# Kernel tuning notes

Measured on AMD Instinct MI355X. Metric: run time of the kernel, lower is better.

## Reference

```python
import jax, jax.numpy as jnp
import numpy as np

NUM_HEADS = 16
HEAD_DIM = 64
HIDDEN = NUM_HEADS * HEAD_DIM  # 1024
MAX_POS = 1024


def setup_inputs() -> dict:
    key = jax.random.key(0)
    ks = jax.random.split(key, 6)
    B, L, H = 8, 1024, HIDDEN
    hidden_states = jax.random.normal(ks[0], (B, L, H), dtype=jnp.float32)
    attention_mask = jnp.zeros((B, 1, 1, L), dtype=jnp.float32)
    scale = 0.02  # keep pre-softmax logits in a sane range
    Wq = jax.random.normal(ks[1], (H, H), dtype=jnp.float32) * scale
    Wk = jax.random.normal(ks[2], (H, H), dtype=jnp.float32) * scale
    Wv = jax.random.normal(ks[3], (H, H), dtype=jnp.float32) * scale
    bq = jnp.zeros((H,), dtype=jnp.float32)
    bk = jnp.zeros((H,), dtype=jnp.float32)
    bv = jnp.zeros((H,), dtype=jnp.float32)
    dist_emb = jax.random.normal(ks[4], (2 * MAX_POS - 1, HEAD_DIM), dtype=jnp.float32) * scale
    return {"hidden_states": hidden_states, "attention_mask": attention_mask,
            "Wq": Wq, "bq": bq, "Wk": Wk, "bk": bk, "Wv": Wv, "bv": bv,
            "dist_emb": dist_emb}


def _split_heads(x):
    # [B, L, H] -> [B, nH, L, hd]
    B, L, _ = x.shape
    return x.reshape(B, L, NUM_HEADS, HEAD_DIM).transpose(0, 2, 1, 3)


def reference(hidden_states, attention_mask, Wq, bq, Wk, bk, Wv, bv, dist_emb):
    B, L, H = hidden_states.shape
    q = _split_heads(hidden_states @ Wq.T + bq)  # [B,h,L,d]
    k = _split_heads(hidden_states @ Wk.T + bk)
    v = _split_heads(hidden_states @ Wv.T + bv)

    scores = jnp.einsum("bhld,bhrd->bhlr", q, k)

    # relative_key_query positional bias
    pos_l = jnp.arange(L)[:, None]
    pos_r = jnp.arange(L)[None, :]
    dist_idx = pos_l - pos_r + MAX_POS - 1          # [L, L], in [0, 2*MAX_POS-2]
    pos_emb = dist_emb[dist_idx]                    # [L, L, d]
    scores = scores + jnp.einsum("bhld,lrd->bhlr", q, pos_emb)
    scores = scores + jnp.einsum("bhrd,lrd->bhlr", k, pos_emb)

    scores = scores / jnp.sqrt(jnp.float32(HEAD_DIM))
    scores = scores + attention_mask                # additive mask broadcast [B,1,1,L]
    probs = jax.nn.softmax(scores, axis=-1)         # dropout = identity (eval)
    ctx = jnp.einsum("bhlr,bhrd->bhld", probs, v)
    ctx = ctx.transpose(0, 2, 1, 3).reshape(B, L, H)
    return ctx
```

## Files before the change

kernel.cpp:

```cpp
#include <hip/hip_runtime.h>
#include <stdint.h>

typedef short s16x8 __attribute__((ext_vector_type(8)));
typedef float f32x4 __attribute__((ext_vector_type(4)));

#define MFMA16(a, b, c) __builtin_amdgcn_mfma_f32_16x16x32_bf16((a), (b), (c), 0, 0, 0)

__device__ __forceinline__ ushort f2b(float f) {
  union { float f; uint32_t u; } x; x.f = f;
  uint32_t r = x.u + 0x7fffu + ((x.u >> 16) & 1u);
  return (ushort)(r >> 16);
}
__device__ __forceinline__ float b2f(ushort s) {
  union { uint32_t u; float f; } x; x.u = ((uint32_t)s) << 16;
  return x.f;
}
__device__ __forceinline__ uint32_t pack2t(float a, float b) {
  return __builtin_amdgcn_perm(__float_as_uint(b), __float_as_uint(a), 0x07060302u);
}

__global__ __launch_bounds__(256) void cast_f32_bf16(const float* __restrict__ src,
                                                     ushort* __restrict__ dst, int n) {
  int i = (blockIdx.x * 256 + threadIdx.x) * 4;
  if (i + 4 <= n) {
    float4 v = *(const float4*)(src + i);
    ushort4 o; o.x = f2b(v.x); o.y = f2b(v.y); o.z = f2b(v.z); o.w = f2b(v.w);
    *(ushort4*)(dst + i) = o;
  }
}

__device__ __forceinline__ void gload16(const void* g, void* l) {
  __builtin_amdgcn_global_load_lds((const __attribute__((address_space(1))) void*)g,
                                   (__attribute__((address_space(3))) void*)l, 16, 0, 0);
}

__global__ __launch_bounds__(256) void qkv_gemm(
    const ushort* __restrict__ hb, const ushort* __restrict__ wb,
    const float* __restrict__ bq, const float* __restrict__ bk, const float* __restrict__ bv,
    ushort* __restrict__ qb, ushort* __restrict__ kb, ushort* __restrict__ vt) {
  __shared__ ushort As[128 * 32];
  __shared__ ushort Bs[128 * 32];
  const int tid = threadIdx.x;
  const int w = tid >> 6, lane = tid & 63, quad = lane >> 4, l16 = lane & 15;
  const int m0 = blockIdx.y * 128, n0 = blockIdx.x * 128;

  const int srow = w * 32 + (lane >> 2);
  const int scol = (lane & 3) * 8;
  const ushort* ga = hb + (size_t)(m0 + srow) * 1024 + scol;
  const ushort* gw = wb + (size_t)(n0 + srow) * 1024 + scol;
  ushort* lA0 = As + (w * 32) * 32;
  ushort* lA1 = As + (w * 32 + 16) * 32;
  ushort* lB0 = Bs + (w * 32) * 32;
  ushort* lB1 = Bs + (w * 32 + 16) * 32;

  f32x4 acc[4][4];
#pragma unroll
  for (int mt = 0; mt < 4; ++mt)
#pragma unroll
    for (int nt = 0; nt < 4; ++nt) acc[mt][nt] = (f32x4){0.f, 0.f, 0.f, 0.f};

  const int wm = (w >> 1) * 64, wn = (w & 1) * 64;

  for (int k0 = 0; k0 < 1024; k0 += 32) {
    gload16(ga + k0, lA0);
    gload16(ga + k0 + 16 * 1024, lA1);
    gload16(gw + k0, lB0);
    gload16(gw + k0 + 16 * 1024, lB1);
    __syncthreads();
    s16x8 af[4], bfr[4];
#pragma unroll
    for (int mt = 0; mt < 4; ++mt)
      af[mt] = *(const s16x8*)(As + (wm + 16 * mt + l16) * 32 + quad * 8);
#pragma unroll
    for (int nt = 0; nt < 4; ++nt)
      bfr[nt] = *(const s16x8*)(Bs + (wn + 16 * nt + l16) * 32 + quad * 8);
#pragma unroll
    for (int mt = 0; mt < 4; ++mt)
#pragma unroll
      for (int nt = 0; nt < 4; ++nt)
        acc[mt][nt] = MFMA16(af[mt], bfr[nt], acc[mt][nt]);
    __syncthreads();
  }

  const int mat = n0 >> 10;
  const float* bias = (mat == 0) ? bq : ((mat == 1) ? bk : bv);
  const int b = m0 >> 10;
#pragma unroll
  for (int mt = 0; mt < 4; ++mt) {
    int mbase = m0 + wm + 16 * mt + 4 * quad;
#pragma unroll
    for (int nt = 0; nt < 4; ++nt) {
      int n = n0 + wn + 16 * nt + l16;
      int o = n & 1023; int hh = o >> 6; int d = o & 63;
      float bsv = bias[o];
#pragma unroll
      for (int reg = 0; reg < 4; ++reg) {
        int l = (mbase + reg) & 1023;
        ushort bx = f2b(acc[mt][nt][reg] + bsv);
        if (mat == 0)      qb[(((size_t)(b * 16 + hh)) * 1024 + l) * 64 + d] = bx;
        else if (mat == 1) kb[(((size_t)(b * 16 + hh)) * 1024 + l) * 64 + d] = bx;
        else               vt[(((size_t)(b * 16 + hh)) * 64 + d) * 1024 + l] = bx;
      }
    }
  }
}

#define KR  0
#define VR  8192
#define ER  16384
#define SER 28672
#define PR  35072

__device__ __forceinline__ const s16x8* fragp(const ushort* base, int row, int cb) {
  return (const s16x8*)(base + row * 64 + ((cb ^ (row & 7)) * 8));
}

__global__ __launch_bounds__(256, 2) void attn_kernel(
    const ushort* __restrict__ qb, const ushort* __restrict__ kb,
    const ushort* __restrict__ vt, const ushort* __restrict__ eb,
    const float* __restrict__ mask, float* __restrict__ out) {
  __shared__ __align__(16) ushort sm[39168];
  const int tid = threadIdx.x;
  const int w = tid >> 6, lane = tid & 63, quad = lane >> 4, l16 = lane & 15;
  const int bh = blockIdx.y, b = bh >> 4, h = bh & 15;
  const int l0 = blockIdx.x * 64;

  const int srow = lane >> 3;
  const int colb = ((lane & 7) ^ srow) * 8;
  const int row0 = w * 8 + srow;

  const ushort* kp = kb + ((size_t)bh * 1024 + row0) * 64 + colb;
  const ushort* vp = vt + ((size_t)bh * 64 + row0) * 1024 + colb;
  const float* maskp = mask + b * 1024 + l16;

  const int p0 = blockIdx.x % 3;

  {
    const ushort* qp = qb + ((size_t)bh * 1024 + l0 + row0) * 64 + colb;
    gload16(qp,         sm + PR + w * 512);
    gload16(qp + 2048,  sm + PR + 2048 + w * 512);
    gload16(kp,         sm + KR + w * 512);
    gload16(kp + 2048,  sm + KR + 2048 + w * 512);
    gload16(vp,         sm + VR + w * 512);
    gload16(vp + 32768, sm + VR + 2048 + w * 512);
    const int t0i = l0 + 960;
#pragma unroll
    for (int c2 = 0; c2 < 4; ++c2) {
      int jb = w * 8 + 32 * c2;
      int seg = p0 + (jb >> 6); if (seg >= 3) seg -= 3;
      int t = t0i + jb + srow; if (t > 2046) t = 2046;
      gload16(eb + (size_t)t * 64 + colb, sm + ER + seg * 4096 + (jb & 63) * 64);
    }
  }
  __syncthreads();

  s16x8 aq0, aq1;
  {
    int r = w * 16 + l16;
    aq0 = *fragp(sm + PR, r, quad);
    aq1 = *fragp(sm + PR, r, quad + 4);
  }

  float rsum[4];
  f32x4 o_acc[4];
#pragma unroll
  for (int r = 0; r < 4; ++r) rsum[r] = 0.f;
#pragma unroll
  for (int nt = 0; nt < 4; ++nt) o_acc[nt] = (f32x4){0.f, 0.f, 0.f, 0.f};

  const float LOG2E = 1.44269504088896f;
  const float SC = 0.125f * LOG2E;

  int s0 = p0;

  for (int it = 0; it < 16; ++it) {
    const int p = it & 1;
    const int r0 = it * 64;
    if (it > 0) __syncthreads();

    {
      const int rn = (r0 + 64) & 1023;
      gload16(kp + rn * 64,        sm + KR + 4096 * (1 - p) + w * 512);
      gload16(kp + rn * 64 + 2048, sm + KR + 4096 * (1 - p) + 2048 + w * 512);
      gload16(vp + rn,             sm + VR + 4096 * (1 - p) + w * 512);
      gload16(vp + rn + 32768,     sm + VR + 4096 * (1 - p) + 2048 + w * 512);
      int pnew = s0 + 2; if (pnew >= 3) pnew -= 3;
      const int tb = l0 + 960 - r0 - 64;
#pragma unroll
      for (int c2 = 0; c2 < 2; ++c2) {
        int o = w * 8 + 32 * c2;
        int t = tb + o + srow; t = t < 0 ? 0 : (t > 2046 ? 2046 : t);
        gload16(eb + (size_t)t * 64 + colb, sm + ER + pnew * 4096 + o * 64);
      }
    }
    float mkv[4];
#pragma unroll
    for (int nt = 0; nt < 4; ++nt) mkv[nt] = maskp[r0 + 16 * nt] * LOG2E;

    const ushort* Kb = sm + KR + 4096 * p;
    const int sA = s0; int sB = s0 + 1; if (sB >= 3) sB -= 3;

    f32x4 zv[4];
#pragma unroll
    for (int nt = 0; nt < 4; ++nt) {
      int r = 16 * nt + l16;
      s16x8 bk0 = *fragp(Kb, r, quad);
      s16x8 bk1 = *fragp(Kb, r, quad + 4);
      f32x4 z = (f32x4){0.f, 0.f, 0.f, 0.f};
      z = MFMA16(aq0, bk0, z);
      z = MFMA16(aq1, bk1, z);
      zv[nt] = z;
    }
    s16x8 ak0, ak1;
    {
      int r = w * 16 + l16;
      ak0 = *fragp(Kb, r, quad);
      ak1 = *fragp(Kb, r, quad + 4);
    }

    f32x4 d1[5];
#pragma unroll
    for (int i = 0; i < 5; ++i) {
      int blk = w + i;
      int seg = (blk & 4) ? sB : sA;
      int row = seg * 64 + (blk & 3) * 16 + l16;
      s16x8 be0 = *fragp(sm + ER, row, quad);
      s16x8 be1 = *fragp(sm + ER, row, quad + 4);
      f32x4 z = (f32x4){0.f, 0.f, 0.f, 0.f};
      z = MFMA16(aq0, be0, z);
      z = MFMA16(aq1, be1, z);
      d1[i] = z;
    }
#pragma unroll
    for (int r = 0; r < 4; ++r) {
      int idx = (quad * 16 + ((4 * quad + r + 15 - l16) & 15)) * 4;
      float bp[5];
#pragma unroll
      for (int i = 0; i < 5; ++i)
        bp[i] = __int_as_float(__builtin_amdgcn_ds_bpermute(idx, __float_as_int(d1[i][r])));
      bool cnd = (4 * quad + r) > l16;
#pragma unroll
      for (int nt = 0; nt < 4; ++nt)
        zv[nt][r] += cnd ? bp[4 - nt] : bp[3 - nt];
    }

#pragma unroll
    for (int i = 0; i < 5; ++i) {
      int blk = 3 - w + i;
      int seg = (blk & 4) ? sB : sA;
      int row = seg * 64 + (blk & 3) * 16 + l16;
      s16x8 be0 = *fragp(sm + ER, row, quad);
      s16x8 be1 = *fragp(sm + ER, row, quad + 4);
      f32x4 z = (f32x4){0.f, 0.f, 0.f, 0.f};
      z = MFMA16(ak0, be0, z);
      z = MFMA16(ak1, be1, z);
      uint2 pk; pk.x = pack2t(z[0], z[1]); pk.y = pack2t(z[2], z[3]);
      *(uint2*)(sm + SER + w * 1600 + (16 * i + l16) * 20 + 4 * quad) = pk;
    }
    __syncthreads();

    const int bb = (w * 16 + 4 * quad + 15 - l16) * 20 + l16;
#pragma unroll
    for (int nt = 0; nt < 4; ++nt) {
#pragma unroll
      for (int reg = 0; reg < 4; ++reg) {
        float z2 = (zv[nt][reg] + b2f(sm[SER + bb + nt * 1600 + reg * 20])) * SC + mkv[nt];
        float pe = exp2f(z2);
        zv[nt][reg] = pe;
        rsum[reg] += pe;
      }
    }

#pragma unroll
    for (int nt = 0; nt < 4; ++nt) {
      int r = 16 * nt + l16;
      int rcb = r >> 3, rlo = r & 7;
#pragma unroll
      for (int reg = 0; reg < 4; ++reg) {
        int l = w * 16 + 4 * quad + reg;
        sm[PR + l * 64 + ((rcb ^ (l & 7)) * 8) + rlo] = f2b(zv[nt][reg]);
      }
    }
    __syncthreads();

    const ushort* Vb = sm + VR + 4096 * p;
#pragma unroll
    for (int kk = 0; kk < 2; ++kk) {
      s16x8 ap = *fragp(sm + PR, w * 16 + l16, kk * 4 + quad);
#pragma unroll
      for (int nt = 0; nt < 4; ++nt) {
        s16x8 bvf = *fragp(Vb, 16 * nt + l16, kk * 4 + quad);
        o_acc[nt] = MFMA16(ap, bvf, o_acc[nt]);
      }
    }

    s0 = (s0 == 0) ? 2 : s0 - 1;
  }

#pragma unroll
  for (int off = 1; off < 16; off <<= 1)
#pragma unroll
    for (int reg = 0; reg < 4; ++reg)
      rsum[reg] += __shfl_xor(rsum[reg], off);

#pragma unroll
  for (int nt = 0; nt < 4; ++nt)
#pragma unroll
    for (int reg = 0; reg < 4; ++reg) {
      int l = l0 + w * 16 + 4 * quad + reg;
      int d = 16 * nt + l16;
      out[((size_t)(b * 1024 + l)) * 1024 + h * 64 + d] = o_acc[nt][reg] / rsum[reg];
    }
}

extern "C" void kernel_launch(void* const* d_in, const int* in_sizes, int n_in,
                              void* d_out, int out_size, void* d_ws, size_t ws_size,
                              hipStream_t stream) {
  const float* hidden = (const float*)d_in[0];
  const float* mask   = (const float*)d_in[1];
  const float* Wq     = (const float*)d_in[2];
  const float* bq     = (const float*)d_in[3];
  const float* Wk     = (const float*)d_in[4];
  const float* bk     = (const float*)d_in[5];
  const float* Wv     = (const float*)d_in[6];
  const float* bv     = (const float*)d_in[7];
  const float* dist   = (const float*)d_in[8];
  float* out = (float*)d_out;

  ushort* ws = (ushort*)d_ws;
  ushort* qb = ws;
  ushort* kb = ws + 8388608;
  ushort* vt = ws + 16777216;
  ushort* hb = ws + 25165824;
  ushort* wb = ws + 33554432;
  ushort* eb = ws + 36700160;

  cast_f32_bf16<<<8192, 256, 0, stream>>>(hidden, hb, 8388608);
  cast_f32_bf16<<<1024, 256, 0, stream>>>(Wq, wb, 1048576);
  cast_f32_bf16<<<1024, 256, 0, stream>>>(Wk, wb + 1048576, 1048576);
  cast_f32_bf16<<<1024, 256, 0, stream>>>(Wv, wb + 2097152, 1048576);
  cast_f32_bf16<<<128, 256, 0, stream>>>(dist, eb, 131008);

  qkv_gemm<<<dim3(24, 64), 256, 0, stream>>>(hb, wb, bq, bk, bv, qb, kb, vt);
  attn_kernel<<<dim3(16, 128), 256, 0, stream>>>(qb, kb, vt, eb, mask, out);
}
```

Before: 388.1 us.

## Hoist LDS addresses, unroll by parity, drop P barrier, add setprio and pk-cvt

Precomputes the swizzled LDS offsets for K, V, E, P and the permute indices once before the main loop. The loop is unrolled by two so the double-buffer parity becomes a compile-time constant. The block barrier between writing P and the PV MFMAs is removed, since each wave reads back only the P rows it wrote itself. MFMA sections are wrapped in s_setprio, and probabilities are converted to bf16 with v_cvt_pk_bf16_f32. This cuts address arithmetic and one barrier per iteration, at the cost of more live registers, which could hurt occupancy at 2 blocks per CU.

```diff
diff --git a/kernel.cpp b/kernel.cpp
--- a/kernel.cpp
+++ b/kernel.cpp
@@ -17,6 +17,11 @@
 }
 __device__ __forceinline__ uint32_t pack2t(float a, float b) {
   return __builtin_amdgcn_perm(__float_as_uint(b), __float_as_uint(a), 0x07060302u);
+}
+__device__ __forceinline__ uint32_t cvtpk(float a, float b) {
+  uint32_t r;
+  asm("v_cvt_pk_bf16_f32 %0, %1, %2" : "=v"(r) : "v"(a), "v"(b));
+  return r;
 }
 
 __global__ __launch_bounds__(256) void cast_f32_bf16(const float* __restrict__ src,
@@ -111,10 +116,6 @@
 #define SER 28672
 #define PR  35072
 
-__device__ __forceinline__ const s16x8* fragp(const ushort* base, int row, int cb) {
-  return (const s16x8*)(base + row * 64 + ((cb ^ (row & 7)) * 8));
-}
-
 __global__ __launch_bounds__(256, 2) void attn_kernel(
     const ushort* __restrict__ qb, const ushort* __restrict__ kb,
     const ushort* __restrict__ vt, const ushort* __restrict__ eb,
@@ -152,14 +153,48 @@
       gload16(eb + (size_t)t * 64 + colb, sm + ER + seg * 4096 + (jb & 63) * 64);
     }
   }
+
+  const int lm7 = l16 & 7;
+  const int swzq = (quad ^ lm7) * 8;
+  int offR0[4], offR1[4];
+#pragma unroll
+  for (int nt = 0; nt < 4; ++nt) {
+    offR0[nt] = (16 * nt + l16) * 64 + swzq;
+    offR1[nt] = offR0[nt] ^ 32;
+  }
+  const int offW0 = (w * 16 + l16) * 64 + swzq;
+  const int offW1 = offW0 ^ 32;
+  const int offPW0 = PR + offW0, offPW1 = PR + offW1;
+  int eoffA[5], eoffB[5]; bool selA[5], selB[5];
+#pragma unroll
+  for (int i = 0; i < 5; ++i) {
+    int ba = w + i, bbk = 3 - w + i;
+    eoffA[i] = ((ba & 3) * 16 + l16) * 64 + swzq;  selA[i] = (ba & 4) != 0;
+    eoffB[i] = ((bbk & 3) * 16 + l16) * 64 + swzq; selB[i] = (bbk & 4) != 0;
+  }
+  int offSW[5];
+#pragma unroll
+  for (int i = 0; i < 5; ++i)
+    offSW[i] = SER + w * 1600 + (16 * i + l16) * 20 + 4 * quad;
+  const int bbF = SER + (w * 16 + 4 * quad + 15 - l16) * 20 + l16;
+  int addrP[4][4];
+#pragma unroll
+  for (int nt = 0; nt < 4; ++nt)
+#pragma unroll
+    for (int reg = 0; reg < 4; ++reg)
+      addrP[nt][reg] = PR + (w * 16 + 4 * quad + reg) * 64
+                     + (((2 * nt + (l16 >> 3)) ^ ((4 * quad + reg) & 7)) * 8) + lm7;
+  int bidx[4]; bool bcnd[4];
+#pragma unroll
+  for (int r = 0; r < 4; ++r) {
+    bidx[r] = (quad * 16 + ((4 * quad + r + 15 - l16) & 15)) * 4;
+    bcnd[r] = (4 * quad + r) > l16;
+  }
+
   __syncthreads();
 
-  s16x8 aq0, aq1;
-  {
-    int r = w * 16 + l16;
-    aq0 = *fragp(sm + PR, r, quad);
-    aq1 = *fragp(sm + PR, r, quad + 4);
-  }
+  const s16x8 aq0 = *(const s16x8*)(sm + offPW0);
+  const s16x8 aq1 = *(const s16x8*)(sm + offPW1);
 
   float rsum[4];
   f32x4 o_acc[4];
@@ -167,135 +202,138 @@
   for (int r = 0; r < 4; ++r) rsum[r] = 0.f;
 #pragma unroll
   for (int nt = 0; nt < 4; ++nt) o_acc[nt] = (f32x4){0.f, 0.f, 0.f, 0.f};
+  const f32x4 ZACC = {0.f, 0.f, 0.f, 0.f};
 
   const float LOG2E = 1.44269504088896f;
   const float SC = 0.125f * LOG2E;
 
   int s0 = p0;
 
-  for (int it = 0; it < 16; ++it) {
-    const int p = it & 1;
-    const int r0 = it * 64;
-    if (it > 0) __syncthreads();
-
-    {
-      const int rn = (r0 + 64) & 1023;
-      gload16(kp + rn * 64,        sm + KR + 4096 * (1 - p) + w * 512);
-      gload16(kp + rn * 64 + 2048, sm + KR + 4096 * (1 - p) + 2048 + w * 512);
-      gload16(vp + rn,             sm + VR + 4096 * (1 - p) + w * 512);
-      gload16(vp + rn + 32768,     sm + VR + 4096 * (1 - p) + 2048 + w * 512);
-      int pnew = s0 + 2; if (pnew >= 3) pnew -= 3;
-      const int tb = l0 + 960 - r0 - 64;
-#pragma unroll
-      for (int c2 = 0; c2 < 2; ++c2) {
-        int o = w * 8 + 32 * c2;
-        int t = tb + o + srow; t = t < 0 ? 0 : (t > 2046 ? 2046 : t);
-        gload16(eb + (size_t)t * 64 + colb, sm + ER + pnew * 4096 + o * 64);
-      }
-    }
-    float mkv[4];
-#pragma unroll
-    for (int nt = 0; nt < 4; ++nt) mkv[nt] = maskp[r0 + 16 * nt] * LOG2E;
-
-    const ushort* Kb = sm + KR + 4096 * p;
-    const int sA = s0; int sB = s0 + 1; if (sB >= 3) sB -= 3;
-
-    f32x4 zv[4];
-#pragma unroll
-    for (int nt = 0; nt < 4; ++nt) {
-      int r = 16 * nt + l16;
-      s16x8 bk0 = *fragp(Kb, r, quad);
-      s16x8 bk1 = *fragp(Kb, r, quad + 4);
-      f32x4 z = (f32x4){0.f, 0.f, 0.f, 0.f};
-      z = MFMA16(aq0, bk0, z);
-      z = MFMA16(aq1, bk1, z);
-      zv[nt] = z;
-    }
-    s16x8 ak0, ak1;
-    {
-      int r = w * 16 + l16;
-      ak0 = *fragp(Kb, r, quad);
-      ak1 = *fragp(Kb, r, quad + 4);
-    }
-
-    f32x4 d1[5];
-#pragma unroll
-    for (int i = 0; i < 5; ++i) {
-      int blk = w + i;
-      int seg = (blk & 4) ? sB : sA;
-      int row = seg * 64 + (blk & 3) * 16 + l16;
-      s16x8 be0 = *fragp(sm + ER, row, quad);
-      s16x8 be1 = *fragp(sm + ER, row, quad + 4);
-      f32x4 z = (f32x4){0.f, 0.f, 0.f, 0.f};
-      z = MFMA16(aq0, be0, z);
-      z = MFMA16(aq1, be1, z);
-      d1[i] = z;
-    }
-#pragma unroll
-    for (int r = 0; r < 4; ++r) {
-      int idx = (quad * 16 + ((4 * quad + r + 15 - l16) & 15)) * 4;
-      float bp[5];
-#pragma unroll
-      for (int i = 0; i < 5; ++i)
-        bp[i] = __int_as_float(__builtin_amdgcn_ds_bpermute(idx, __float_as_int(d1[i][r])));
-      bool cnd = (4 * quad + r) > l16;
-#pragma unroll
-      for (int nt = 0; nt < 4; ++nt)
-        zv[nt][r] += cnd ? bp[4 - nt] : bp[3 - nt];
-    }
-
-#pragma unroll
-    for (int i = 0; i < 5; ++i) {
-      int blk = 3 - w + i;
-      int seg = (blk & 4) ? sB : sA;
-      int row = seg * 64 + (blk & 3) * 16 + l16;
-      s16x8 be0 = *fragp(sm + ER, row, quad);
-      s16x8 be1 = *fragp(sm + ER, row, quad + 4);
-      f32x4 z = (f32x4){0.f, 0.f, 0.f, 0.f};
-      z = MFMA16(ak0, be0, z);
-      z = MFMA16(ak1, be1, z);
-      uint2 pk; pk.x = pack2t(z[0], z[1]); pk.y = pack2t(z[2], z[3]);
-      *(uint2*)(sm + SER + w * 1600 + (16 * i + l16) * 20 + 4 * quad) = pk;
-    }
-    __syncthreads();
-
-    const int bb = (w * 16 + 4 * quad + 15 - l16) * 20 + l16;
-#pragma unroll
-    for (int nt = 0; nt < 4; ++nt) {
-#pragma unroll
-      for (int reg = 0; reg < 4; ++reg) {
-        float z2 = (zv[nt][reg] + b2f(sm[SER + bb + nt * 1600 + reg * 20])) * SC + mkv[nt];
-        float pe = exp2f(z2);
-        zv[nt][reg] = pe;
-        rsum[reg] += pe;
-      }
-    }
-
-#pragma unroll
-    for (int nt = 0; nt < 4; ++nt) {
-      int r = 16 * nt + l16;
-      int rcb = r >> 3, rlo = r & 7;
-#pragma unroll
-      for (int reg = 0; reg < 4; ++reg) {
-        int l = w * 16 + 4 * quad + reg;
-        sm[PR + l * 64 + ((rcb ^ (l & 7)) * 8) + rlo] = f2b(zv[nt][reg]);
-      }
-    }
-    __syncthreads();
-
-    const ushort* Vb = sm + VR + 4096 * p;
-#pragma unroll
-    for (int kk = 0; kk < 2; ++kk) {
-      s16x8 ap = *fragp(sm + PR, w * 16 + l16, kk * 4 + quad);
-#pragma unroll
-      for (int nt = 0; nt < 4; ++nt) {
-        s16x8 bvf = *fragp(Vb, 16 * nt + l16, kk * 4 + quad);
-        o_acc[nt] = MFMA16(ap, bvf, o_acc[nt]);
-      }
-    }
-
-    s0 = (s0 == 0) ? 2 : s0 - 1;
-  }
+#define ATTN_ITER(P)                                                               \
+  {                                                                                \
+    const int it = 2 * ith + (P);                                                  \
+    const int r0 = it * 64;                                                        \
+    __syncthreads();      \
+                   \
+    {                                                                              \
+      const int rn = (r0 + 64) & 1023;                                             \
+      gload16(kp + rn * 64,        sm + KR + 4096 * (1 - (P)) + w * 512);          \
+      gload16(kp + rn * 64 + 2048, sm + KR + 4096 * (1 - (P)) + 2048 + w * 512);   \
+      gload16(vp + rn,             sm + VR + 4096 * (1 - (P)) + w * 512);          \
+      gload16(vp + rn + 32768,     sm + VR + 4096 * (1 - (P)) + 2048 + w * 512);   \
+      int pnew = s0 + 2; if (pnew >= 3) pnew -= 3;                                 \
+      const int tb = l0 + 960 - r0 - 64;                                           \
+      _Pragma("unroll")                                                            \
+      for (int c2 = 0; c2 < 2; ++c2) {                                             \
+        int o = w * 8 + 32 * c2;                                                   \
+        int t = tb + o + srow; t = t < 0 ? 0 : (t > 2046 ? 2046 : t);              \
+        gload16(eb + (size_t)t * 64 + colb, sm + ER + pnew * 4096 + o * 64);       \
+      }                                                                            \
+    }                                                                              \
+    float mkv[4];                                                                  \
+    _Pragma("unroll")                                                              \
+    for (int nt = 0; nt < 4; ++nt) mkv[nt] = maskp[r0 + 16 * nt] * LOG2E;          \
+    const int sA4 = s0 * 4096;                                                     \
+    int sBi = s0 + 1; if (sBi >= 3) sBi -= 3;                                      \
+    const int sB4 = sBi * 4096;                                                    \
+    const ushort* KbP = sm + KR + 4096 * (P);                                      \
+                         \
+    __builtin_amdgcn_s_setprio(1);                                                 \
+    f32x4 zv[4];                                                                   \
+    _Pragma("unroll")                                                              \
+    for (int nt = 0; nt < 4; ++nt) {                                               \
+      s16x8 bk0 = *(const s16x8*)(KbP + offR0[nt]);                                \
+      s16x8 bk1 = *(const s16x8*)(KbP + offR1[nt]);                                \
+      f32x4 z = MFMA16(aq0, bk0, ZACC);                                            \
+      zv[nt] = MFMA16(aq1, bk1, z);                                                \
+    }                                                                              \
+    const s16x8 ak0 = *(const s16x8*)(KbP + offW0);                                \
+    const s16x8 ak1 = *(const s16x8*)(KbP + offW1);                                \
+    f32x4 d1[5];                                                                   \
+    _Pragma("unroll")                                                              \
+    for (int i = 0; i < 5; ++i) {                                                  \
+      int ea = (selA[i] ? sB4 : sA4) + eoffA[i];                                   \
+      s16x8 be0 = *(const s16x8*)(sm + ER + ea);                                   \
+      s16x8 be1 = *(const s16x8*)(sm + ER + (ea ^ 32));                            \
+      f32x4 z = MFMA16(aq0, be0, ZACC);                                            \
+      d1[i] = MFMA16(aq1, be1, z);                                                 \
+    }                                                                              \
+    __builtin_amdgcn_s_setprio(0);                                                 \
+                                  \
+    _Pragma("unroll")                                                              \
+    for (int r = 0; r < 4; ++r) {                                                  \
+      float bp[5];                                                                 \
+      _Pragma("unroll")                                                            \
+      for (int i = 0; i < 5; ++i)                                                  \
+        bp[i] = __int_as_float(                                                    \
+            __builtin_amdgcn_ds_bpermute(bidx[r], __float_as_int(d1[i][r])));      \
+      _Pragma("unroll")                                                            \
+      for (int nt = 0; nt < 4; ++nt)                                               \
+        zv[nt][r] += bcnd[r] ? bp[4 - nt] : bp[3 - nt];                            \
+    }                                                                              \
+                               \
+    __builtin_amdgcn_s_setprio(1);                                                 \
+    _Pragma("unroll")                                                              \
+    for (int i = 0; i < 5; ++i) {                                                  \
+      int ea = (selB[i] ? sB4 : sA4) + eoffB[i];                                   \
+      s16x8 be0 = *(const s16x8*)(sm + ER + ea);                                   \
+      s16x8 be1 = *(const s16x8*)(sm + ER + (ea ^ 32));                            \
+      f32x4 z = MFMA16(ak0, be0, ZACC);                                            \
+      z = MFMA16(ak1, be1, z);                                                     \
+      uint2 pk; pk.x = pack2t(z[0], z[1]); pk.y = pack2t(z[2], z[3]);              \
+      *(uint2*)(sm + offSW[i]) = pk;                                               \
+    }                                                                              \
+    __builtin_amdgcn_s_setprio(0);                                                 \
+    __syncthreads();                  \
+                    \
+    _Pragma("unroll")                                                              \
+    for (int nt = 0; nt < 4; ++nt) {                                               \
+      _Pragma("unroll")                                                            \
+      for (int reg = 0; reg < 4; ++reg) {                                          \
+        float z2 = (zv[nt][reg] + b2f(sm[bbF + nt * 1600 + reg * 20])) * SC        \
+                 + mkv[nt];                                                        \
+        float pe = exp2f(z2);                                                      \
+        zv[nt][reg] = pe;                                                          \
+        rsum[reg] += pe;                                                           \
+      }                                                                            \
+    }                                                                              \
+               \
+    _Pragma("unroll")                                                              \
+    for (int nt = 0; nt < 4; ++nt) {                                               \
+      uint32_t u01 = cvtpk(zv[nt][0], zv[nt][1]);                                  \
+      uint32_t u23 = cvtpk(zv[nt][2], zv[nt][3]);                                  \
+      sm[addrP[nt][0]] = (ushort)u01;                                              \
+      sm[addrP[nt][1]] = (ushort)(u01 >> 16);                                      \
+      sm[addrP[nt][2]] = (ushort)u23;                                              \
+      sm[addrP[nt][3]] = (ushort)(u23 >> 16);                                      \
+    }                                                                              \
+       \
+    __builtin_amdgcn_s_setprio(1);                                                 \
+    {                                                                              \
+      const ushort* VbP = sm + VR + 4096 * (P);                                    \
+      const s16x8 ap0 = *(const s16x8*)(sm + offPW0);                              \
+      _Pragma("unroll")                                                            \
+      for (int nt = 0; nt < 4; ++nt) {                                             \
+        s16x8 bv0 = *(const s16x8*)(VbP + offR0[nt]);                              \
+        o_acc[nt] = MFMA16(ap0, bv0, o_acc[nt]);                                   \
+      }                                                                            \
+      const s16x8 ap1 = *(const s16x8*)(sm + offPW1);                              \
+      _Pragma("unroll")                                                            \
+      for (int nt = 0; nt < 4; ++nt) {                                             \
+        s16x8 bv1 = *(const s16x8*)(VbP + offR1[nt]);                              \
+        o_acc[nt] = MFMA16(ap1, bv1, o_acc[nt]);                                   \
+      }                                                                            \
+    }                                                                              \
+    __builtin_amdgcn_s_setprio(0);                                                 \
+    s0 = (s0 == 0) ? 2 : s0 - 1;                   \
+  }
+
+#pragma unroll 1
+  for (int ith = 0; ith < 8; ++ith) {
+    ATTN_ITER(0)
+    ATTN_ITER(1)
+  }
+#undef ATTN_ITER
 
 #pragma unroll
   for (int off = 1; off < 16; off <<= 1)
```

Measured after the change: 382.7 us. Within noise of the previous version (-1.4%).
